# Performance work log

Measured on AMD Instinct MI355X. Metric: run time of the kernel, lower is better.

## Reference

```python
import jax, jax.numpy as jnp
import numpy as np

K = 3; STRIDE = 1; PAD = 1
IN_C = 256; OUT_C = 512
SPAN = K * K * IN_C        # 2304, im2col row count
M = 3                      # ALSH augmentation dims
TABLE_SIZE = 8             # hash buckets
R = 2.5                    # LSH bin width


def setup_inputs() -> dict:
    key = jax.random.key(0)
    k1, k2, k3, k4 = jax.random.split(key, 4)
    stdv = 1.0 / np.sqrt(SPAN)
    inp = jax.random.normal(k1, (16, IN_C, 56, 56), dtype=jnp.float32)
    kernels = jax.random.uniform(k2, (OUT_C, SPAN), minval=-stdv, maxval=stdv,
                                 dtype=jnp.float32)
    a_hash = jax.random.normal(k3, (SPAN + M,), dtype=jnp.float32)
    b_hash = jax.random.uniform(k4, (1,), dtype=jnp.float32) * R
    return {"input": inp, "kernels": kernels, "a_hash": a_hash,
            "b_hash": b_hash, "mode": 1}


def _P(x, m):
    # ALSH P-augmentation: append ||x||^(2^i), i=1..m, per row. x: [O, SPAN]
    n = jnp.linalg.norm(x, axis=1, keepdims=True)
    ext = jnp.concatenate([n ** (2 ** (i + 1)) for i in range(m)], axis=1)
    return jnp.concatenate([x, ext], axis=1)  # [O, SPAN+M]


def _bucket(vals, b, r, ts):
    # floor((v+b)/r) ; fmod ts ; abs  (matches torch fmod-then-abs semantics)
    idx = jnp.floor((vals + b) / r).astype(jnp.int32)
    return jnp.abs(jnp.fmod(idx, ts))


def _im2col_matr(x):
    # [N, C, H, W] -> [SPAN, N*H2*W2]
    n = x.shape[0]
    h2 = (x.shape[2] - K + 2 * PAD) // STRIDE + 1
    w2 = (x.shape[3] - K + 2 * PAD) // STRIDE + 1
    patches = jax.lax.conv_general_dilated_patches(
        x, (K, K), (STRIDE, STRIDE), [(PAD, PAD), (PAD, PAD)])  # [N, SPAN, H2, W2]
    return patches.reshape(n, SPAN, h2 * w2).transpose(1, 0, 2).reshape(SPAN, -1), h2, w2


def reference(input, kernels, a_hash, b_hash, mode):
    n = input.shape[0]
    patch_matr, h2, w2 = _im2col_matr(input)  # [SPAN, L]

    # ---- build ALSH table: bucket of each kernel row ----
    kvals = _P(kernels, M) @ a_hash           # [OUT_C]
    kbuck = _bucket(kvals, b_hash[0], R, TABLE_SIZE)

    # ---- vote: hash every unit-normalized patch column, take modal bucket ----
    unit = patch_matr / jnp.linalg.norm(patch_matr, axis=0, keepdims=True)
    q_ext = jnp.full((M, unit.shape[1]), 0.5, dtype=unit.dtype)
    votes = a_hash @ jnp.concatenate([unit, q_ext], axis=0)  # [L]
    vbuck = _bucket(votes, b_hash[0], R, TABLE_SIZE)
    counts = jnp.bincount(vbuck, length=TABLE_SIZE)
    bucket = int(jnp.argmax(counts))

    # ---- gather active kernel rows for that bucket (data-dependent) ----
    rows = np.sort(np.where(np.asarray(kbuck) == bucket)[0])
    if rows.size != 0:
        active = kernels[jnp.asarray(rows)]          # [oc, SPAN]
        out = active @ patch_matr                    # [oc, L]
        if mode:
            out = out / (float(rows.size) / OUT_C)
        oc = int(rows.size)
    else:
        out = kernels @ patch_matr
        oc = OUT_C

    out = out.reshape(oc, n, h2 * w2).transpose(1, 0, 2).reshape(n, oc, h2, w2)
    return (out, jnp.asarray(rows, dtype=jnp.int32))
```

## Files before the change

kernel.cpp:

```cpp
#include <hip/hip_runtime.h>
#include <math.h>

#define N_    16
#define C_    256
#define H_    56
#define W_    56
#define HW_   3136
#define NPIX  50176
#define OUTC  512
#define SPAN_ 2304
#define BLKPX 256
#define HBYTES 24576

typedef unsigned short u16;
typedef unsigned int   u32;
typedef __attribute__((ext_vector_type(8))) short bf16x8;
typedef __attribute__((ext_vector_type(8))) unsigned short u16x8;
typedef __attribute__((ext_vector_type(4))) float f32x4;
typedef __attribute__((ext_vector_type(4))) unsigned short u16x4;

__device__ __forceinline__ u16 f2bf(float v) {
    u32 x = __float_as_uint(v);
    u32 r = (x + 0x7fffu + ((x >> 16) & 1u)) >> 16;
    return (u16)r;
}

__device__ __forceinline__ int bucketf(float v, float b) {
    int idx = (int)floorf((v + b) / 2.5f);
    int r = idx % 8;
    return r < 0 ? -r : r;
}

__global__ void kbucket_kernel(const float* __restrict__ kern,
                               const float* __restrict__ ah,
                               const float* __restrict__ bh,
                               int* __restrict__ kbuck) {
    int oc = blockIdx.x;
    const float* kr = kern + (size_t)oc * SPAN_;
    float dot = 0.f, ss = 0.f;
    for (int j = threadIdx.x; j < SPAN_; j += 64) {
        float kv = kr[j];
        dot += kv * ah[j];
        ss  += kv * kv;
    }
    for (int o = 32; o; o >>= 1) {
        dot += __shfl_down(dot, o);
        ss  += __shfl_down(ss, o);
    }
    if (threadIdx.x == 0) {
        float n2 = ss;
        float n4 = n2 * n2;
        float n8 = n4 * n4;
        float v = dot + n2 * ah[SPAN_] + n4 * ah[SPAN_ + 1] + n8 * ah[SPAN_ + 2];
        kbuck[oc] = bucketf(v, bh[0]);
    }
}

__global__ __launch_bounds__(256) void prep_fused(const float* __restrict__ x,
                                                  const float* __restrict__ ah,
                                                  u16* __restrict__ xp,
                                                  float* __restrict__ g,
                                                  float* __restrict__ s2) {
    __shared__ float aL[SPAN_];
    __shared__ u16 tl[64][68];
    __shared__ float red[4][64][10];
    int t = threadIdx.x;
    for (int j = t; j < SPAN_; j += 256) aL[j] = ah[j];

    int px0 = blockIdx.x * 64;
    int img = px0 / HW_;
    int hw0 = px0 - img * HW_;
    int px_l = t & 63;
    int cq   = t >> 6;
    float pg[9];
#pragma unroll
    for (int kk = 0; kk < 9; ++kk) pg[kk] = 0.f;
    float ps = 0.f;
    __syncthreads();

    for (int cb0 = 0; cb0 < 4; ++cb0) {
        int c0 = cb0 * 64;
#pragma unroll
        for (int rep = 0; rep < 16; ++rep) {
            int c_l = rep * 4 + cq;
            float v = x[((size_t)(img * C_ + c0 + c_l)) * HW_ + hw0 + px_l];
            tl[px_l][c_l] = f2bf(v);
            const float* ac = &aL[(c0 + c_l) * 9];
#pragma unroll
            for (int kk = 0; kk < 9; ++kk) pg[kk] += ac[kk] * v;
            ps += v * v;
        }
        __syncthreads();
        int c4  = t & 15;
        int pxs = t >> 4;
#pragma unroll
        for (int rep = 0; rep < 4; ++rep) {
            int pl = rep * 16 + pxs;
            u16x4 v4 = *(const u16x4*)(&tl[pl][c4 * 4]);
            *(u16x4*)(&xp[((size_t)(px0 + pl)) * C_ + c0 + c4 * 4]) = v4;
        }
        __syncthreads();
    }

#pragma unroll
    for (int kk = 0; kk < 9; ++kk) red[cq][px_l][kk] = pg[kk];
    red[cq][px_l][9] = ps;
    __syncthreads();
    for (int it = t; it < 640; it += 256) {
        int pl = it / 10;
        int j  = it - pl * 10;
        float s = red[0][pl][j] + red[1][pl][j] + red[2][pl][j] + red[3][pl][j];
        int q = px0 + pl;
        if (j < 9) g[(size_t)j * NPIX + q] = s;
        else       s2[q] = s;
    }
}

__global__ __launch_bounds__(256) void vote_kernel(const float* __restrict__ g,
                                                   const float* __restrict__ s2,
                                                   const float* __restrict__ ah,
                                                   const float* __restrict__ bh,
                                                   int* __restrict__ counts) {
    __shared__ int hist[8];
    if (threadIdx.x < 8) hist[threadIdx.x] = 0;
    __syncthreads();
    int q = blockIdx.x * 256 + threadIdx.x;
    int n = q / HW_;
    int p = q - n * HW_;
    int h = p / W_;
    int w = p - h * W_;
    float dot = 0.f, ss = 0.f;
#pragma unroll
    for (int kk = 0; kk < 9; ++kk) {
        int dh = kk / 3 - 1, dw = kk % 3 - 1;
        int hh = h + dh, ww = w + dw;
        if (hh >= 0 && hh < H_ && ww >= 0 && ww < W_) {
            int idx = n * HW_ + hh * W_ + ww;
            dot += g[(size_t)kk * NPIX + idx];
            ss  += s2[idx];
        }
    }
    float qext = 0.5f * (ah[SPAN_] + ah[SPAN_ + 1] + ah[SPAN_ + 2]);
    float v = dot / sqrtf(ss) + qext;
    int b = bucketf(v, bh[0]);
    atomicAdd(&hist[b], 1);
    __syncthreads();
    if (threadIdx.x < 8) atomicAdd(&counts[threadIdx.x], hist[threadIdx.x]);
}

__global__ __launch_bounds__(512) void select_kernel(const int* __restrict__ counts,
                                                     const int* __restrict__ kbuck,
                                                     int* __restrict__ rowsb,
                                                     int* __restrict__ meta,
                                                     float* __restrict__ out,
                                                     int oc_total) {
    __shared__ int sBest;
    __shared__ int sScan[512];
    int t = threadIdx.x;
    if (t == 0) {
        int best = 0, bc = counts[0];
        for (int i = 1; i < 8; ++i) {
            int c = counts[i];
            if (c > bc) { bc = c; best = i; }
        }
        sBest = best;
    }
    __syncthreads();
    int best = sBest;
    int flag = (kbuck[t] == best) ? 1 : 0;
    sScan[t] = flag;
    __syncthreads();
    for (int off = 1; off < 512; off <<= 1) {
        int add = (t >= off) ? sScan[t - off] : 0;
        __syncthreads();
        sScan[t] += add;
        __syncthreads();
    }
    int cnt = sScan[511];
    int pos = sScan[t] - flag;
    if (flag) rowsb[pos] = t;
    if (cnt == 0) rowsb[t] = t;
    else if (t >= cnt) rowsb[t] = 0;
    if (t == 0) {
        meta[0] = cnt;
        meta[1] = (cnt == 0) ? OUTC : cnt;
    }
    float* rout = out + (size_t)N_ * oc_total * HW_;
    int eff = (cnt == 0) ? OUTC : cnt;
    int nw = eff < oc_total ? eff : oc_total;
    if (cnt == 0) {
        if (t < nw) rout[t] = (float)t;
    } else if (flag && pos < nw) {
        rout[pos] = (float)t;
    }
}

__global__ __launch_bounds__(256) void prep_w(const float* __restrict__ kern,
                                              const int* __restrict__ rowsb,
                                              const int* __restrict__ meta,
                                              const int* __restrict__ mode,
                                              u16* __restrict__ wfrag, int nf4) {
    int e = blockIdx.x * 256 + threadIdx.x;
    int lane = e & 63;
    int t2 = e >> 6;
    int g = t2 % nf4;
    int s = t2 / nf4;
    int kk = s >> 3;
    int cb = s & 7;
    int q = lane >> 4;
    int mcol = lane & 15;
    int ocEff = meta[1];
    int cnt = meta[0];
    float scale = (mode[0] && cnt > 0) ? 512.0f / (float)cnt : 1.0f;
    int oc_i = g * 16 + mcol;
    bool valid = oc_i < ocEff;
    int row = valid ? rowsb[oc_i] : 0;
    const float* kr = kern + (size_t)row * SPAN_;
    u16 w8[8];
#pragma unroll
    for (int j = 0; j < 8; ++j) {
        int c = cb * 32 + q * 8 + j;
        float v = valid ? kr[c * 9 + kk] * scale : 0.f;
        w8[j] = f2bf(v);
    }
    u16* dst = wfrag + ((size_t)((s * nf4 + g) * 64 + lane)) * 8;
#pragma unroll
    for (int j = 0; j < 8; ++j) dst[j] = w8[j];
}

__global__ __launch_bounds__(256, 2) void conv_mfma(const u16* __restrict__ xp,
                                                    const u16* __restrict__ wfrag,
                                                    float* __restrict__ out,
                                                    int nf4, int oc_total, int nby) {
    __shared__ char halo[2 * HBYTES];

    int flat = blockIdx.x;
    int bx, by;
    int full = 192 * nby;
    if (flat < full) {
        int gsz = 8 * nby;
        int gi = flat / gsz;
        int tr = flat - gi * gsz;
        by = tr >> 3;
        bx = gi * 8 + (tr & 7);
    } else {
        int tr = flat - full;
        by = tr >> 2;
        bx = 192 + (tr & 3);
    }

    const int t = threadIdx.x;
    const int lane = t & 63;
    const int wv = t >> 6;
    const int pb = bx * BLKPX;
    const int fb = by * 4;
    const int lane15 = lane & 15;
    const int laneq  = lane >> 4;

    int hA[4], wA[4], aBase[4];
#pragma unroll
    for (int f = 0; f < 4; ++f) {
        int p = pb + wv * 64 + f * 16 + lane15;
        int img = p / HW_;
        int rp = p - img * HW_;
        hA[f] = rp / W_;
        wA[f] = rp - hA[f] * W_;
        aBase[f] = (57 + wv * 64 + f * 16 + lane15) * 64 + laneq * 16;
    }

    f32x4 acc[4][4];
#pragma unroll
    for (int f = 0; f < 4; ++f)
#pragma unroll
        for (int gg = 0; gg < 4; ++gg) acc[f][gg] = (f32x4){0.f, 0.f, 0.f, 0.f};
    const bf16x8 zf = {0, 0, 0, 0, 0, 0, 0, 0};

    const char* xpb = (const char*)xp;
    const char* gsrc[6];
#pragma unroll
    for (int r = 0; r < 6; ++r) {
        int p = pb - 57 + r * 64 + (t >> 2);
        p = p < 0 ? 0 : (p >= NPIX ? NPIX - 1 : p);
        gsrc[r] = xpb + (size_t)p * 512 + (t & 3) * 16;
    }

#pragma unroll
    for (int r = 0; r < 6; ++r)
        __builtin_amdgcn_global_load_lds(
            (const __attribute__((address_space(1))) unsigned int*)(gsrc[r]),
            (__attribute__((address_space(3))) unsigned int*)&halo[r * 4096 + t * 16],
            16, 0, 0);

    const size_t kkStride = (size_t)8 * nf4 * 512;

    for (int cb = 0; cb < 8; ++cb) {
        __syncthreads();
        const char* hb = &halo[(cb & 1) * HBYTES];

        if (cb < 7) {
            char* hn = &halo[((cb + 1) & 1) * HBYTES];
#pragma unroll
            for (int r = 0; r < 6; ++r)
                __builtin_amdgcn_global_load_lds(
                    (const __attribute__((address_space(1))) unsigned int*)
                        (gsrc[r] + (cb + 1) * 64),
                    (__attribute__((address_space(3))) unsigned int*)
                        &hn[r * 4096 + t * 16],
                    16, 0, 0);
        }

        const u16* wcb = wfrag + ((size_t)cb * nf4 + fb) * 512 + lane * 8;
        bf16x8 bW[4];
#pragma unroll
        for (int gg = 0; gg < 4; ++gg)
            bW[gg] = *(const bf16x8*)(wcb + (size_t)gg * 512);

#pragma unroll
        for (int kk = 0; kk < 9; ++kk) {
            bf16x8 bWn[4];
            if (kk < 8) {
                const u16* wn = wcb + (size_t)(kk + 1) * kkStride;
#pragma unroll
                for (int gg = 0; gg < 4; ++gg)
                    bWn[gg] = *(const bf16x8*)(wn + (size_t)gg * 512);
            }
            const int dh = kk / 3 - 1, dw = kk % 3 - 1;
            const int toff = (dh * W_ + dw) * 64;
            bf16x8 aX[4];
#pragma unroll
            for (int f = 0; f < 4; ++f) {
                int hh = hA[f] + dh, ww = wA[f] + dw;
                bool val = (hh >= 0) & (hh < H_) & (ww >= 0) & (ww < W_);
                bf16x8 a = *(const bf16x8*)&hb[aBase[f] + toff];
                aX[f] = val ? a : zf;
            }
#pragma unroll
            for (int gg = 0; gg < 4; ++gg)
#pragma unroll
                for (int f = 0; f < 4; ++f)
                    acc[f][gg] = __builtin_amdgcn_mfma_f32_16x16x32_bf16(
                        aX[f], bW[gg], acc[f][gg], 0, 0, 0);
            if (kk < 8) {
#pragma unroll
                for (int gg = 0; gg < 4; ++gg) bW[gg] = bWn[gg];
            }
        }
    }

#pragma unroll
    for (int f = 0; f < 4; ++f) {
        int p0 = pb + wv * 64 + f * 16 + laneq * 4;
        int img0 = p0 / HW_;
        int hw0 = p0 - img0 * HW_;
#pragma unroll
        for (int gg = 0; gg < 4; ++gg) {
            int oc = (fb + gg) * 16 + lane15;
            if (oc < oc_total) {
                float* op = out + ((size_t)img0 * oc_total + oc) * HW_ + hw0;
                *(f32x4*)op = acc[f][gg];
            }
        }
    }
}

extern "C" void kernel_launch(void* const* d_in, const int* in_sizes, int n_in,
                              void* d_out, int out_size, void* d_ws, size_t ws_size,
                              hipStream_t stream) {
    const float* x    = (const float*)d_in[0];
    const float* kern = (const float*)d_in[1];
    const float* ah   = (const float*)d_in[2];
    const float* bh   = (const float*)d_in[3];
    const int*   mode = (const int*)d_in[4];
    float* out = (float*)d_out;

    int oc_total = (out_size % (N_ * HW_ + 1) == 0) ? out_size / (N_ * HW_ + 1)
                                                    : OUTC;
    int nfTot = (oc_total + 15) / 16;
    int nf4   = ((nfTot + 3) / 4) * 4;
    int nby   = nf4 / 4;

    u16*   xp     = (u16*)d_ws;
    u16*   wfrag  = xp + (size_t)NPIX * C_;
    float* g      = (float*)(wfrag + (size_t)72 * 32 * 64 * 8);
    float* s2     = g + (size_t)9 * NPIX;
    int*   counts = (int*)(s2 + NPIX);
    int*   kbuck  = counts + 8;
    int*   rowsb  = kbuck + OUTC;
    int*   meta   = rowsb + OUTC;

    hipMemsetAsync(counts, 0, 8 * sizeof(int), stream);

    prep_fused<<<NPIX / 64, 256, 0, stream>>>(x, ah, xp, g, s2);

    kbucket_kernel<<<OUTC, 64, 0, stream>>>(kern, ah, bh, kbuck);
    vote_kernel<<<NPIX / 256, 256, 0, stream>>>(g, s2, ah, bh, counts);
    select_kernel<<<1, 512, 0, stream>>>(counts, kbuck, rowsb, meta, out, oc_total);

    prep_w<<<18 * nf4, 256, 0, stream>>>(kern, rowsb, meta, mode, wfrag, nf4);

    conv_mfma<<<(NPIX / BLKPX) * nby, 256, 0, stream>>>(xp, wfrag, out, nf4,
                                                        oc_total, nby);
}
```

Measured before the change: 109.5 us.

## Swizzle LDS halo, precompute tap validity masks, triple-buffer weight fragments

```diff
diff --git a/kernel.cpp b/kernel.cpp
--- a/kernel.cpp
+++ b/kernel.cpp
@@ -11,6 +11,7 @@
 #define SPAN_ 2304
 #define BLKPX 256
 #define HBYTES 24576
+#define ZOFF  (2 * HBYTES)
 
 typedef unsigned short u16;
 typedef unsigned int   u32;
@@ -228,11 +229,11 @@
     for (int j = 0; j < 8; ++j) dst[j] = w8[j];
 }
 
-__global__ __launch_bounds__(256, 2) void conv_mfma(const u16* __restrict__ xp,
+__global__ __launch_bounds__(256, 3) void conv_mfma(const u16* __restrict__ xp,
                                                     const u16* __restrict__ wfrag,
                                                     float* __restrict__ out,
                                                     int nf4, int oc_total, int nby) {
-    __shared__ char halo[2 * HBYTES];
+    __shared__ char halo[2 * HBYTES + 64];
 
     int flat = blockIdx.x;
     int bx, by;
@@ -257,15 +258,30 @@
     const int lane15 = lane & 15;
     const int laneq  = lane >> 4;
 
-    int hA[4], wA[4], aBase[4];
+    if (t < 4) *(u16x8*)&halo[ZOFF + t * 16] = (u16x8){0,0,0,0,0,0,0,0};
+
+    u32 valMask[4];
+    int aB[4][3];
 #pragma unroll
     for (int f = 0; f < 4; ++f) {
         int p = pb + wv * 64 + f * 16 + lane15;
         int img = p / HW_;
         int rp = p - img * HW_;
-        hA[f] = rp / W_;
-        wA[f] = rp - hA[f] * W_;
-        aBase[f] = (57 + wv * 64 + f * 16 + lane15) * 64 + laneq * 16;
+        int h = rp / W_;
+        int w = rp - h * W_;
+        u32 m = 0;
+#pragma unroll
+        for (int kk = 0; kk < 9; ++kk) {
+            int dh = kk / 3 - 1, dw = kk % 3 - 1;
+            int hh = h + dh, ww = w + dw;
+            if (hh >= 0 && hh < H_ && ww >= 0 && ww < W_) m |= (1u << kk);
+        }
+        valMask[f] = m;
+#pragma unroll
+        for (int j = 0; j < 3; ++j) {
+            int sn = 57 + wv * 64 + f * 16 + lane15 + (j - 1);
+            aB[f][j] = sn * 64 + ((laneq ^ ((sn >> 1) & 3)) << 4);
+        }
     }
 
     f32x4 acc[4][4];
@@ -273,79 +289,77 @@
     for (int f = 0; f < 4; ++f)
 #pragma unroll
         for (int gg = 0; gg < 4; ++gg) acc[f][gg] = (f32x4){0.f, 0.f, 0.f, 0.f};
-    const bf16x8 zf = {0, 0, 0, 0, 0, 0, 0, 0};
 
     const char* xpb = (const char*)xp;
-    const char* gsrc[6];
+    const int q4 = (((t & 3) ^ ((t >> 3) & 3)) << 4);
+    int gpx[6];
 #pragma unroll
     for (int r = 0; r < 6; ++r) {
         int p = pb - 57 + r * 64 + (t >> 2);
-        p = p < 0 ? 0 : (p >= NPIX ? NPIX - 1 : p);
-        gsrc[r] = xpb + (size_t)p * 512 + (t & 3) * 16;
+        gpx[r] = p < 0 ? 0 : (p >= NPIX ? NPIX - 1 : p);
     }
 
 #pragma unroll
     for (int r = 0; r < 6; ++r)
         __builtin_amdgcn_global_load_lds(
-            (const __attribute__((address_space(1))) unsigned int*)(gsrc[r]),
+            (const __attribute__((address_space(1))) unsigned int*)
+                (xpb + (size_t)gpx[r] * 512 + q4),
             (__attribute__((address_space(3))) unsigned int*)&halo[r * 4096 + t * 16],
             16, 0, 0);
 
-    const size_t kkStride = (size_t)8 * nf4 * 512;
+    const size_t cbStride = (size_t)nf4 * 512;
+    const size_t kkStride = cbStride * 8;
+    const u16* wl = wfrag + (size_t)fb * 512 + (size_t)lane * 8;
+    bf16x8 bB[3][4];
+#define LOADB(slot, cb_, kk_) do {                                              \
+    const u16* _wp = wl + (size_t)(kk_) * kkStride + (size_t)(cb_) * cbStride;  \
+    _Pragma("unroll")                                                           \
+    for (int _g = 0; _g < 4; ++_g)                                              \
+        bB[slot][_g] = *(const bf16x8*)(_wp + (size_t)_g * 512);                \
+} while (0)
+
+    LOADB(0, 0, 0);
+    LOADB(1, 0, 1);
 
     for (int cb = 0; cb < 8; ++cb) {
         __syncthreads();
-        const char* hb = &halo[(cb & 1) * HBYTES];
+        const int hoff = (cb & 1) * HBYTES;
 
         if (cb < 7) {
-            char* hn = &halo[((cb + 1) & 1) * HBYTES];
+            const int nb = ((cb + 1) & 1) * HBYTES;
 #pragma unroll
             for (int r = 0; r < 6; ++r)
                 __builtin_amdgcn_global_load_lds(
                     (const __attribute__((address_space(1))) unsigned int*)
-                        (gsrc[r] + (cb + 1) * 64),
+                        (xpb + (size_t)gpx[r] * 512 + (cb + 1) * 64 + q4),
                     (__attribute__((address_space(3))) unsigned int*)
-                        &hn[r * 4096 + t * 16],
+                        &halo[nb + r * 4096 + t * 16],
                     16, 0, 0);
         }
 
-        const u16* wcb = wfrag + ((size_t)cb * nf4 + fb) * 512 + lane * 8;
-        bf16x8 bW[4];
-#pragma unroll
-        for (int gg = 0; gg < 4; ++gg)
-            bW[gg] = *(const bf16x8*)(wcb + (size_t)gg * 512);
-
 #pragma unroll
         for (int kk = 0; kk < 9; ++kk) {
-            bf16x8 bWn[4];
-            if (kk < 8) {
-                const u16* wn = wcb + (size_t)(kk + 1) * kkStride;
-#pragma unroll
-                for (int gg = 0; gg < 4; ++gg)
-                    bWn[gg] = *(const bf16x8*)(wn + (size_t)gg * 512);
-            }
-            const int dh = kk / 3 - 1, dw = kk % 3 - 1;
-            const int toff = (dh * W_ + dw) * 64;
+            if (kk < 7)            LOADB((kk + 2) % 3, cb, kk + 2);
+            else if (cb < 7)       LOADB((kk + 2) % 3, cb + 1, kk - 7);
+
+            const int dh = kk / 3 - 1;
+            const int j  = kk % 3;
+            const int toffH = hoff + dh * 3584;
             bf16x8 aX[4];
 #pragma unroll
             for (int f = 0; f < 4; ++f) {
-                int hh = hA[f] + dh, ww = wA[f] + dw;
-                bool val = (hh >= 0) & (hh < H_) & (ww >= 0) & (ww < W_);
-                bf16x8 a = *(const bf16x8*)&hb[aBase[f] + toff];
-                aX[f] = val ? a : zf;
+                int addr = ((valMask[f] >> kk) & 1) ? (aB[f][j] + toffH) : ZOFF;
+                aX[f] = *(const bf16x8*)&halo[addr];
             }
 #pragma unroll
             for (int gg = 0; gg < 4; ++gg)
 #pragma unroll
                 for (int f = 0; f < 4; ++f)
                     acc[f][gg] = __builtin_amdgcn_mfma_f32_16x16x32_bf16(
-                        aX[f], bW[gg], acc[f][gg], 0, 0, 0);
-            if (kk < 8) {
-#pragma unroll
-                for (int gg = 0; gg < 4; ++gg) bW[gg] = bWn[gg];
-            }
-        }
-    }
+                        aX[f], bB[kk % 3][gg], acc[f][gg], 0, 0, 0);
+        }
+    }
+#undef LOADB
 
 #pragma unroll
     for (int f = 0; f < 4; ++f) {
```

After: 113.5 us. 3.6% more time.
